# Kernel tuning notes

Measured on AMD Instinct MI355X. Metric: run time of the kernel, lower is better.

## Reference

```python
import jax, jax.numpy as jnp
import numpy as np

EPS = 1e-08


def _cdist(x):
    # x: [B, N, D] -> [B, N, N] Euclidean distances, safe-sqrt for grad at 0
    diff = x[:, :, None, :] - x[:, None, :, :]          # [B, N, N, D]
    sq = jnp.sum(diff * diff, axis=-1)                   # [B, N, N]
    pos = sq > 0
    return jnp.where(pos, jnp.sqrt(jnp.where(pos, sq, 1.0)), 0.0)


def setup_inputs() -> dict:
    key = jax.random.key(0)
    k1, k2, k3 = jax.random.split(key, 3)
    B, N, D = 32, 1024, 3
    preds = jax.random.normal(k1, (B, N, D), dtype=jnp.float32)
    targets = jax.random.normal(k2, (B, N, D), dtype=jnp.float32)
    mask = jax.random.randint(k3, (B, N), 0, 2, dtype=jnp.int32)
    return {"preds": preds, "targets": targets, "mask": mask}


def reference(preds, targets, mask):
    m = mask.astype(preds.dtype)                         # [B, N]
    diag_att = m[:, :, None] * m[:, None, :]            # [B, N, N]
    dist_preds = _cdist(preds)                           # [B, N, N]
    dist_targets = _cdist(targets)                       # [B, N, N]
    dist = jnp.abs(dist_preds - dist_targets) / (dist_targets + EPS)  # relative=True
    loss = dist * diag_att
    return loss.sum() / diag_att.sum()
```

## Files before the change

### kernel.cpp

```cpp
#include <hip/hip_runtime.h>


constexpr int   NT    = 256;
constexpr int   ROWCH = 32;
constexpr int   SUBS  = ROWCH * 2;
constexpr int   RBLK  = 4;
constexpr float EPS   = 1e-8f;

__global__ __launch_bounds__(NT) void idl_main(
    const float* __restrict__ preds, const float* __restrict__ targets,
    const int* __restrict__ mask, float* __restrict__ partials,
    float* __restrict__ counts, int N)
{
    const int bid      = blockIdx.x;
    const int b        = bid / SUBS;
    const int sub      = bid % SUBS;
    const int rowBase  = (sub >> 1) * 32;
    const int colBase  = (sub & 1) * 512;

    __shared__ float scpx[512], scpy[512], scpz[512];
    __shared__ float sctx[512], scty[512], sctz[512];
    __shared__ int   s_rows[32];
    __shared__ int   s_nrows, s_cnt;
    __shared__ float s_red[NT / 64];

    const float* pb = preds   + (size_t)b * N * 3;
    const float* tb = targets + (size_t)b * N * 3;
    const int*   mb = mask    + (size_t)b * N;
    const int    tid = threadIdx.x;

    if (tid == 0) s_cnt = 0;
    __syncthreads();

    for (int j = colBase + tid; j < colBase + 512; j += NT) {
        if (mb[j] != 0) {
            int p = atomicAdd(&s_cnt, 1);
            scpx[p] = pb[j * 3 + 0]; scpy[p] = pb[j * 3 + 1]; scpz[p] = pb[j * 3 + 2];
            sctx[p] = tb[j * 3 + 0]; scty[p] = tb[j * 3 + 1]; sctz[p] = tb[j * 3 + 2];
        }
    }
    if (tid < 64) {
        bool act = (tid < 32) && (mb[rowBase + tid] != 0);
        unsigned long long bal = __ballot(act);
        if (act) {
            int pos = __popcll(bal & ((1ull << tid) - 1ull));
            s_rows[pos] = rowBase + tid;
        }
        if (tid == 0) s_nrows = (int)__popcll(bal);
    }
    __syncthreads();

    const int Kc    = s_cnt;
    const int nrows = s_nrows;

    float acc = 0.0f;
    for (int rg = 0; rg < nrows; rg += RBLK) {
        float rpx[RBLK], rpy[RBLK], rpz[RBLK];
        float rtx[RBLK], rty[RBLK], rtz[RBLK];
        bool  rv[RBLK];
#pragma unroll
        for (int k = 0; k < RBLK; ++k) {
            const int rr = rg + k;
            rv[k] = rr < nrows;
            const int i = rv[k] ? s_rows[rr] : s_rows[0];
            rpx[k] = pb[i * 3 + 0]; rpy[k] = pb[i * 3 + 1]; rpz[k] = pb[i * 3 + 2];
            rtx[k] = tb[i * 3 + 0]; rty[k] = tb[i * 3 + 1]; rtz[k] = tb[i * 3 + 2];
        }
        for (int j = tid; j < Kc; j += NT) {
            const float jpx = scpx[j], jpy = scpy[j], jpz = scpz[j];
            const float jtx = sctx[j], jty = scty[j], jtz = sctz[j];
#pragma unroll
            for (int k = 0; k < RBLK; ++k) {
                if (rv[k]) {
                    float dx = jpx - rpx[k], dy = jpy - rpy[k], dz = jpz - rpz[k];
                    float sp = fmaf(dx, dx, fmaf(dy, dy, dz * dz));
                    float dp = __builtin_amdgcn_sqrtf(sp);
                    float ex = jtx - rtx[k], ey = jty - rty[k], ez = jtz - rtz[k];
                    float st = fmaf(ex, ex, fmaf(ey, ey, ez * ez));
                    float dt = __builtin_amdgcn_sqrtf(st);
                    acc = fmaf(fabsf(dp - dt), __builtin_amdgcn_rcpf(dt + EPS), acc);
                }
            }
        }
    }

    for (int off = 32; off > 0; off >>= 1)
        acc += __shfl_down(acc, off, 64);
    if ((tid & 63) == 0) s_red[tid >> 6] = acc;
    __syncthreads();
    if (tid == 0) {
        float s = 0.0f;
#pragma unroll
        for (int w = 0; w < NT / 64; ++w) s += s_red[w];
        partials[bid] = s;
    }

    if (sub == 0) {
        __shared__ int s_ri[NT / 64];
        int c = 0;
        for (int i = tid; i < N; i += NT) c += (mb[i] != 0);
        for (int off = 32; off > 0; off >>= 1)
            c += __shfl_down(c, off, 64);
        if ((tid & 63) == 0) s_ri[tid >> 6] = c;
        __syncthreads();
        if (tid == 0) {
            int t = 0;
#pragma unroll
            for (int w = 0; w < NT / 64; ++w) t += s_ri[w];
            counts[b] = (float)t;
        }
    }
}

__global__ __launch_bounds__(256) void idl_final(
    const float* __restrict__ partials, int nP,
    const float* __restrict__ counts, int B, float* __restrict__ out)
{
    __shared__ float s_n[4], s_d[4];
    const int tid = threadIdx.x;
    float num = 0.0f, den = 0.0f;
    for (int i = tid; i < nP; i += 256) num += partials[i];
    for (int i = tid; i < B;  i += 256) { float c = counts[i]; den = fmaf(c, c, den); }
    for (int off = 32; off > 0; off >>= 1) {
        num += __shfl_down(num, off, 64);
        den += __shfl_down(den, off, 64);
    }
    if ((tid & 63) == 0) { s_n[tid >> 6] = num; s_d[tid >> 6] = den; }
    __syncthreads();
    if (tid == 0) {
        float n = 0.0f, d = 0.0f;
#pragma unroll
        for (int w = 0; w < 4; ++w) { n += s_n[w]; d += s_d[w]; }
        out[0] = n / d;
    }
}

__global__ __launch_bounds__(NT) void idl_fb(
    const float* __restrict__ preds, const float* __restrict__ targets,
    const int* __restrict__ mask, float* __restrict__ ws, int N)
{
    const int b     = blockIdx.x / 32;
    const int chunk = blockIdx.x % 32;
    __shared__ float spx[1024], spy[1024], spz[1024];
    __shared__ float stx[1024], sty[1024], stz[1024];
    __shared__ int   s_rows[32];
    __shared__ int   s_nrows, s_cnt;
    const float* pb = preds   + (size_t)b * N * 3;
    const float* tb = targets + (size_t)b * N * 3;
    const int*   mb = mask    + (size_t)b * N;
    const int tid = threadIdx.x;
    if (tid == 0) s_cnt = 0;
    __syncthreads();
    for (int j = tid; j < N; j += NT) {
        if (mb[j] != 0) {
            int p = atomicAdd(&s_cnt, 1);
            spx[p] = pb[j*3+0]; spy[p] = pb[j*3+1]; spz[p] = pb[j*3+2];
            stx[p] = tb[j*3+0]; sty[p] = tb[j*3+1]; stz[p] = tb[j*3+2];
        }
    }
    if (tid < 64) {
        bool act = (tid < 32) && (mb[chunk * 32 + tid] != 0);
        unsigned long long bal = __ballot(act);
        if (act) s_rows[__popcll(bal & ((1ull << tid) - 1ull))] = chunk * 32 + tid;
        if (tid == 0) s_nrows = (int)__popcll(bal);
    }
    __syncthreads();
    const int K = s_cnt, nrows = s_nrows;
    float acc = 0.0f;
    for (int rg = 0; rg < nrows; ++rg) {
        const int i = s_rows[rg];
        float rpx = pb[i*3+0], rpy = pb[i*3+1], rpz = pb[i*3+2];
        float rtx = tb[i*3+0], rty = tb[i*3+1], rtz = tb[i*3+2];
        for (int j = tid; j < K; j += NT) {
            float dx = spx[j]-rpx, dy = spy[j]-rpy, dz = spz[j]-rpz;
            float dp = __builtin_amdgcn_sqrtf(fmaf(dx,dx,fmaf(dy,dy,dz*dz)));
            float ex = stx[j]-rtx, ey = sty[j]-rty, ez = stz[j]-rtz;
            float dt = __builtin_amdgcn_sqrtf(fmaf(ex,ex,fmaf(ey,ey,ez*ez)));
            acc = fmaf(fabsf(dp-dt), __builtin_amdgcn_rcpf(dt + EPS), acc);
        }
    }
    for (int off = 32; off > 0; off >>= 1) acc += __shfl_down(acc, off, 64);
    if ((tid & 63) == 0) atomicAdd(&ws[0], acc);
    if (chunk == 0 && tid == 0) atomicAdd(&ws[1], (float)K * (float)K);
}
__global__ void idl_fb_final(const float* __restrict__ ws, float* __restrict__ out)
{ out[0] = ws[0] / ws[1]; }

extern "C" void kernel_launch(void* const* d_in, const int* in_sizes, int n_in,
                              void* d_out, int out_size, void* d_ws, size_t ws_size,
                              hipStream_t stream)
{
    const float* preds   = (const float*)d_in[0];
    const float* targets = (const float*)d_in[1];
    const int*   mask    = (const int*)d_in[2];
    const int N = 1024;
    const int B = in_sizes[2] / N;
    const int nBlocks = B * SUBS;
    const size_t need = (size_t)(nBlocks + B) * sizeof(float);

    if (ws_size >= need) {
        float* partials = (float*)d_ws;
        float* counts   = partials + nBlocks;
        idl_main<<<dim3(nBlocks), NT, 0, stream>>>(preds, targets, mask, partials, counts, N);
        idl_final<<<dim3(1), 256, 0, stream>>>(partials, nBlocks, counts, B, (float*)d_out);
    } else {
        float* ws = (float*)d_ws;
        hipMemsetAsync(ws, 0, 2 * sizeof(float), stream);
        idl_fb<<<dim3(B * 32), NT, 0, stream>>>(preds, targets, mask, ws, N);
        idl_fb_final<<<dim3(1), 1, 0, stream>>>(ws, (float*)d_out);
    }
}
```

Measured before the change: 20.01 us.

## Precompact masked points and balance row work across blocks with fused final reduction

Adds a per-batch compaction kernel that writes masked preds/targets to workspace in SoA layout. The pair kernel then splits the compacted rows evenly across blocks instead of using fixed 32-row windows with variable active counts. The final reduction is folded into the pair kernel through atomics and a last-block counter, removing a launch. This trades an extra serial low-parallelism compaction kernel and global atomics for better load balance.

```diff
diff --git a/kernel.cpp b/kernel.cpp
--- a/kernel.cpp
+++ b/kernel.cpp
@@ -1,137 +1,151 @@
 #include <hip/hip_runtime.h>
 
 
-constexpr int   NT    = 256;
-constexpr int   ROWCH = 32;
-constexpr int   SUBS  = ROWCH * 2;
-constexpr int   RBLK  = 4;
-constexpr float EPS   = 1e-8f;
-
-__global__ __launch_bounds__(NT) void idl_main(
+constexpr int   NT     = 256;
+constexpr int   NMAX   = 1024;
+constexpr int   ROWCH  = 32;
+constexpr int   HALVES = 2;
+constexpr int   SUBS   = ROWCH * HALVES;
+constexpr int   RBLK   = 4;
+constexpr float EPS    = 1e-8f;
+
+constexpr int WS_NUM  = 0;
+constexpr int WS_DONE = 1;
+constexpr int WS_FCNT = 8;
+constexpr int WS_KCNT = 8 + 256;
+constexpr int WS_DATA = 1024;
+
+__global__ __launch_bounds__(NT) void idl_compact(
     const float* __restrict__ preds, const float* __restrict__ targets,
-    const int* __restrict__ mask, float* __restrict__ partials,
-    float* __restrict__ counts, int N)
-{
-    const int bid      = blockIdx.x;
-    const int b        = bid / SUBS;
-    const int sub      = bid % SUBS;
-    const int rowBase  = (sub >> 1) * 32;
-    const int colBase  = (sub & 1) * 512;
-
-    __shared__ float scpx[512], scpy[512], scpz[512];
-    __shared__ float sctx[512], scty[512], sctz[512];
-    __shared__ int   s_rows[32];
-    __shared__ int   s_nrows, s_cnt;
-    __shared__ float s_red[NT / 64];
-
+    const int* __restrict__ mask, float* __restrict__ ws, int N)
+{
+    const int b = blockIdx.x, tid = threadIdx.x;
+    const int wid = tid >> 6, lane = tid & 63;
+    __shared__ int s_wt[NT / 64];
+    __shared__ int s_base;
+
+    if (tid == 0) s_base = 0;
+    if (b == 0 && tid < 2) ws[tid] = 0.0f;
+
+    const int*   mb = mask    + (size_t)b * N;
     const float* pb = preds   + (size_t)b * N * 3;
     const float* tb = targets + (size_t)b * N * 3;
-    const int*   mb = mask    + (size_t)b * N;
-    const int    tid = threadIdx.x;
-
-    if (tid == 0) s_cnt = 0;
-    __syncthreads();
-
-    for (int j = colBase + tid; j < colBase + 512; j += NT) {
-        if (mb[j] != 0) {
-            int p = atomicAdd(&s_cnt, 1);
-            scpx[p] = pb[j * 3 + 0]; scpy[p] = pb[j * 3 + 1]; scpz[p] = pb[j * 3 + 2];
-            sctx[p] = tb[j * 3 + 0]; scty[p] = tb[j * 3 + 1]; sctz[p] = tb[j * 3 + 2];
-        }
-    }
-    if (tid < 64) {
-        bool act = (tid < 32) && (mb[rowBase + tid] != 0);
-        unsigned long long bal = __ballot(act);
+    float*       db = ws + WS_DATA + (size_t)b * 6 * NMAX;
+    __syncthreads();
+
+    for (int r = 0; r < N; r += NT) {
+        const int  idx = r + tid;
+        const bool act = (idx < N) && (mb[idx] != 0);
+        const unsigned long long bal = __ballot(act);
+        if (lane == 0) s_wt[wid] = (int)__popcll(bal);
+        __syncthreads();
+        int woff = s_base;
+        for (int w = 0; w < wid; ++w) woff += s_wt[w];
+        int total = 0;
+#pragma unroll
+        for (int w = 0; w < NT / 64; ++w) total += s_wt[w];
         if (act) {
-            int pos = __popcll(bal & ((1ull << tid) - 1ull));
-            s_rows[pos] = rowBase + tid;
-        }
-        if (tid == 0) s_nrows = (int)__popcll(bal);
-    }
-    __syncthreads();
-
-    const int Kc    = s_cnt;
-    const int nrows = s_nrows;
+            const int pos = woff + (int)__popcll(bal & ((1ull << lane) - 1ull));
+            db[0 * NMAX + pos] = pb[idx * 3 + 0];
+            db[1 * NMAX + pos] = pb[idx * 3 + 1];
+            db[2 * NMAX + pos] = pb[idx * 3 + 2];
+            db[3 * NMAX + pos] = tb[idx * 3 + 0];
+            db[4 * NMAX + pos] = tb[idx * 3 + 1];
+            db[5 * NMAX + pos] = tb[idx * 3 + 2];
+        }
+        __syncthreads();
+        if (tid == 0) s_base += total;
+        __syncthreads();
+    }
+    if (tid == 0) {
+        const int K = s_base;
+        ((int*)ws)[WS_KCNT + b] = K;
+        ws[WS_FCNT + b] = (float)K;
+    }
+}
+
+__global__ __launch_bounds__(NT) void idl_pairs(
+    float* __restrict__ ws, float* __restrict__ out, int B, int nBlocks)
+{
+    const int bid = blockIdx.x;
+    const int b   = bid / SUBS;
+    const int sub = bid % SUBS;
+    const int rc  = sub >> 1;
+    const int h   = sub & 1;
+    const int tid = threadIdx.x;
+
+    __shared__ float sx[512], sy[512], sz[512];
+    __shared__ float qx[512], qy[512], qz[512];
+    __shared__ float s_red[NT / 64];
+
+    const int    K  = ((const int*)ws)[WS_KCNT + b];
+    const float* db = ws + WS_DATA + (size_t)b * 6 * NMAX;
+
+    const int c0 = h * 512;
+    const int nc = max(min(c0 + 512, K) - c0, 0);
+    for (int j = tid; j < nc; j += NT) {
+        sx[j] = db[0 * NMAX + c0 + j];
+        sy[j] = db[1 * NMAX + c0 + j];
+        sz[j] = db[2 * NMAX + c0 + j];
+        qx[j] = db[3 * NMAX + c0 + j];
+        qy[j] = db[4 * NMAX + c0 + j];
+        qz[j] = db[5 * NMAX + c0 + j];
+    }
+    __syncthreads();
+
+    const int rpc = (K + ROWCH - 1) / ROWCH;
+    const int r0  = rc * rpc;
+    const int r1  = min(r0 + rpc, K);
 
     float acc = 0.0f;
-    for (int rg = 0; rg < nrows; rg += RBLK) {
+    for (int rg = r0; rg < r1; rg += RBLK) {
         float rpx[RBLK], rpy[RBLK], rpz[RBLK];
         float rtx[RBLK], rty[RBLK], rtz[RBLK];
         bool  rv[RBLK];
 #pragma unroll
         for (int k = 0; k < RBLK; ++k) {
             const int rr = rg + k;
-            rv[k] = rr < nrows;
-            const int i = rv[k] ? s_rows[rr] : s_rows[0];
-            rpx[k] = pb[i * 3 + 0]; rpy[k] = pb[i * 3 + 1]; rpz[k] = pb[i * 3 + 2];
-            rtx[k] = tb[i * 3 + 0]; rty[k] = tb[i * 3 + 1]; rtz[k] = tb[i * 3 + 2];
-        }
-        for (int j = tid; j < Kc; j += NT) {
-            const float jpx = scpx[j], jpy = scpy[j], jpz = scpz[j];
-            const float jtx = sctx[j], jty = scty[j], jtz = sctz[j];
+            rv[k] = rr < r1;
+            const int i = rv[k] ? rr : r0;
+            rpx[k] = db[0 * NMAX + i]; rpy[k] = db[1 * NMAX + i]; rpz[k] = db[2 * NMAX + i];
+            rtx[k] = db[3 * NMAX + i]; rty[k] = db[4 * NMAX + i]; rtz[k] = db[5 * NMAX + i];
+        }
+        for (int j = tid; j < nc; j += NT) {
+            const float jpx = sx[j], jpy = sy[j], jpz = sz[j];
+            const float jtx = qx[j], jty = qy[j], jtz = qz[j];
 #pragma unroll
             for (int k = 0; k < RBLK; ++k) {
                 if (rv[k]) {
                     float dx = jpx - rpx[k], dy = jpy - rpy[k], dz = jpz - rpz[k];
-                    float sp = fmaf(dx, dx, fmaf(dy, dy, dz * dz));
-                    float dp = __builtin_amdgcn_sqrtf(sp);
+                    float dp = __builtin_amdgcn_sqrtf(fmaf(dx, dx, fmaf(dy, dy, dz * dz)));
                     float ex = jtx - rtx[k], ey = jty - rty[k], ez = jtz - rtz[k];
-                    float st = fmaf(ex, ex, fmaf(ey, ey, ez * ez));
-                    float dt = __builtin_amdgcn_sqrtf(st);
+                    float dt = __builtin_amdgcn_sqrtf(fmaf(ex, ex, fmaf(ey, ey, ez * ez)));
                     acc = fmaf(fabsf(dp - dt), __builtin_amdgcn_rcpf(dt + EPS), acc);
                 }
             }
         }
     }
 
-    for (int off = 32; off > 0; off >>= 1)
-        acc += __shfl_down(acc, off, 64);
+    for (int off = 32; off > 0; off >>= 1) acc += __shfl_down(acc, off, 64);
     if ((tid & 63) == 0) s_red[tid >> 6] = acc;
     __syncthreads();
     if (tid == 0) {
         float s = 0.0f;
 #pragma unroll
         for (int w = 0; w < NT / 64; ++w) s += s_red[w];
-        partials[bid] = s;
-    }
-
-    if (sub == 0) {
-        __shared__ int s_ri[NT / 64];
-        int c = 0;
-        for (int i = tid; i < N; i += NT) c += (mb[i] != 0);
-        for (int off = 32; off > 0; off >>= 1)
-            c += __shfl_down(c, off, 64);
-        if ((tid & 63) == 0) s_ri[tid >> 6] = c;
-        __syncthreads();
-        if (tid == 0) {
-            int t = 0;
-#pragma unroll
-            for (int w = 0; w < NT / 64; ++w) t += s_ri[w];
-            counts[b] = (float)t;
-        }
-    }
-}
-
-__global__ __launch_bounds__(256) void idl_final(
-    const float* __restrict__ partials, int nP,
-    const float* __restrict__ counts, int B, float* __restrict__ out)
-{
-    __shared__ float s_n[4], s_d[4];
-    const int tid = threadIdx.x;
-    float num = 0.0f, den = 0.0f;
-    for (int i = tid; i < nP; i += 256) num += partials[i];
-    for (int i = tid; i < B;  i += 256) { float c = counts[i]; den = fmaf(c, c, den); }
-    for (int off = 32; off > 0; off >>= 1) {
-        num += __shfl_down(num, off, 64);
-        den += __shfl_down(den, off, 64);
-    }
-    if ((tid & 63) == 0) { s_n[tid >> 6] = num; s_d[tid >> 6] = den; }
-    __syncthreads();
-    if (tid == 0) {
-        float n = 0.0f, d = 0.0f;
-#pragma unroll
-        for (int w = 0; w < 4; ++w) { n += s_n[w]; d += s_d[w]; }
-        out[0] = n / d;
+        atomicAdd(&ws[WS_NUM], s);
+        __threadfence();
+        const unsigned t = atomicAdd((unsigned*)ws + WS_DONE, 1u);
+        if (t == (unsigned)(nBlocks - 1)) {
+            __threadfence();
+            const float num = atomicAdd(&ws[WS_NUM], 0.0f);
+            float den = 0.0f;
+            for (int bb = 0; bb < B; ++bb) {
+                const float c = ws[WS_FCNT + bb];
+                den = fmaf(c, c, den);
+            }
+            out[0] = num / den;
+        }
     }
 }
 
@@ -195,16 +209,15 @@
     const int*   mask    = (const int*)d_in[2];
     const int N = 1024;
     const int B = in_sizes[2] / N;
-    const int nBlocks = B * SUBS;
-    const size_t need = (size_t)(nBlocks + B) * sizeof(float);
-
-    if (ws_size >= need) {
-        float* partials = (float*)d_ws;
-        float* counts   = partials + nBlocks;
-        idl_main<<<dim3(nBlocks), NT, 0, stream>>>(preds, targets, mask, partials, counts, N);
-        idl_final<<<dim3(1), 256, 0, stream>>>(partials, nBlocks, counts, B, (float*)d_out);
+    float* ws = (float*)d_ws;
+
+    const int    nBlocks = B * SUBS;
+    const size_t need    = ((size_t)WS_DATA + (size_t)B * 6 * NMAX) * sizeof(float);
+
+    if (ws_size >= need && B <= 256) {
+        idl_compact<<<dim3(B),       NT, 0, stream>>>(preds, targets, mask, ws, N);
+        idl_pairs  <<<dim3(nBlocks), NT, 0, stream>>>(ws, (float*)d_out, B, nBlocks);
     } else {
-        float* ws = (float*)d_ws;
         hipMemsetAsync(ws, 0, 2 * sizeof(float), stream);
         idl_fb<<<dim3(B * 32), NT, 0, stream>>>(preds, targets, mask, ws, N);
         idl_fb_final<<<dim3(1), 1, 0, stream>>>(ws, (float*)d_out);
```

After: 64.98 us. 225% more time.
